# Kernel tuning notes

Measured on AMD Instinct MI355X. Metric: run time of the kernel, lower is better.

## Reference

```python
import jax, jax.numpy as jnp
import numpy as np

N_NODES = 100000
N_EDGES = 3200000
EMBED_DIM = 64


def setup_inputs() -> dict:
    key = jax.random.key(0)
    k1, k2, k3, k4 = jax.random.split(key, 4)
    x = jax.random.normal(k1, (N_NODES, EMBED_DIM), dtype=jnp.float32)
    adj_rows = jax.random.randint(k2, (N_EDGES,), 0, N_NODES, dtype=jnp.int64)
    adj_cols = jax.random.randint(k3, (N_EDGES,), 0, N_NODES, dtype=jnp.int64)
    adj_vals = jax.random.uniform(k4, (N_EDGES,), dtype=jnp.float32)
    return {"x": x, "adj_rows": adj_rows, "adj_cols": adj_cols, "adj_vals": adj_vals}


def reference(x, adj_rows, adj_cols, adj_vals):
    # out = adj @ x, adj sparse COO: out[r] += v * x[c] for each (r, c, v)
    messages = x[adj_cols] * adj_vals[:, None]          # [E, D]
    out = jax.ops.segment_sum(messages, adj_rows, num_segments=N_NODES)  # [N, D]
    return out
```

## Files before the change

kernel.cpp:

```cpp
#include <hip/hip_runtime.h>
#include <hip/hip_fp16.h>

#define EMBED_DIM 64
#define NBMAX 1024
#define RPB 128
#define RPB_SHIFT 7
#define CAP 6144
#define CHUNK 8192
#define SCAT_T 512
#define EPT (CHUNK / SCAT_T)
#define SENTINEL_KEY 0xFFFFFFFFu
#define SCAT_LDS (NBMAX * 4 * 3 + 512 * 4 + CHUNK * 8)

typedef float f32x8 __attribute__((ext_vector_type(8)));
typedef float f32x4 __attribute__((ext_vector_type(4)));

__device__ __forceinline__ int load_idx(const void* p, int e, bool i64) {
    return i64 ? (int)((const long long*)p)[e] : ((const int*)p)[e];
}

static inline size_t align_up(size_t v, size_t a) { return (v + a - 1) & ~(a - 1); }

__global__ __launch_bounds__(1024) void detect_zero_kernel(
    const unsigned int* __restrict__ rows_u32, int* __restrict__ flag,
    int* __restrict__ gcur, int nb) {
    const int tid = threadIdx.x;
    if (tid == 0) {
        int nz = 0;
        for (int i = 1; i < 128; i += 2) nz += (rows_u32[i] != 0u);
        *flag = (nz == 0) ? 1 : 0;
    }
    if (tid < nb) gcur[tid] = 0;
}

__global__ __launch_bounds__(256) void xconv_kernel(
    const float* __restrict__ x, ushort* __restrict__ xh, int n8) {
    int i = blockIdx.x * 256 + threadIdx.x;
    if (i >= n8) return;
    float4 a = ((const float4*)x)[i * 2];
    float4 b = ((const float4*)x)[i * 2 + 1];
    ushort h[8];
    h[0] = __half_as_ushort(__float2half_rn(a.x));
    h[1] = __half_as_ushort(__float2half_rn(a.y));
    h[2] = __half_as_ushort(__float2half_rn(a.z));
    h[3] = __half_as_ushort(__float2half_rn(a.w));
    h[4] = __half_as_ushort(__float2half_rn(b.x));
    h[5] = __half_as_ushort(__float2half_rn(b.y));
    h[6] = __half_as_ushort(__float2half_rn(b.z));
    h[7] = __half_as_ushort(__float2half_rn(b.w));
    ((uint4*)xh)[i] = *(const uint4*)h;
}

__global__ __launch_bounds__(SCAT_T) void bscatter_kernel(
    const void* __restrict__ rows_p, const void* __restrict__ cols_p,
    const float* __restrict__ vals, int* __restrict__ gcur,
    uint2* __restrict__ recs, const int* __restrict__ flag_p,
    int n_edges, int nb) {
    extern __shared__ char smem[];
    int*   h     = (int*)smem;
    int*   gbase = h + NBMAX;
    int*   lbase = gbase + NBMAX;
    int*   tsum  = lbase + NBMAX;
    uint2* rec   = (uint2*)(tsum + 512);

    const bool i64 = (*flag_p != 0);
    const int tid = threadIdx.x;
    const int c0e = blockIdx.x * CHUNK;
    int rloc[EPT];

    for (int i = tid; i < NBMAX; i += SCAT_T) h[i] = 0;
    __syncthreads();

    #pragma unroll
    for (int k = 0; k < EPT; ++k) {
        int e = c0e + k * SCAT_T + tid;
        int r = (e < n_edges) ? load_idx(rows_p, e, i64) : -1;
        rloc[k] = r;
        if (r >= 0) atomicAdd(&h[r >> RPB_SHIFT], 1);
    }
    __syncthreads();

    const int b0 = 2 * tid, b1 = 2 * tid + 1;
    int cb0 = h[b0], cb1 = h[b1];
    int s = cb0 + cb1;
    tsum[tid] = s;
    __syncthreads();
    for (int d = 1; d < 512; d <<= 1) {
        int u = (tid >= d) ? tsum[tid - d] : 0;
        __syncthreads();
        tsum[tid] += u;
        __syncthreads();
    }
    {
        int run = tsum[tid] - s;
        lbase[b0] = run;
        lbase[b1] = run + cb0;
        int a0 = (cb0 + 7) & ~7, a1 = (cb1 + 7) & ~7;
        gbase[b0] = cb0 ? (b0 * CAP + atomicAdd(&gcur[b0], a0)) : 0;
        gbase[b1] = cb1 ? (b1 * CAP + atomicAdd(&gcur[b1], a1)) : 0;
        h[b0] = 0;
        h[b1] = 0;
    }
    __syncthreads();

    #pragma unroll
    for (int k0 = 0; k0 < EPT; k0 += 4) {
        int cc[4]; float vv[4];
        #pragma unroll
        for (int j = 0; j < 4; ++j) {
            int e = c0e + (k0 + j) * SCAT_T + tid;
            if (rloc[k0 + j] >= 0) {
                cc[j] = load_idx(cols_p, e, i64);
                vv[j] = vals[e];
            }
        }
        #pragma unroll
        for (int j = 0; j < 4; ++j) {
            int r = rloc[k0 + j];
            if (r >= 0) {
                int b = r >> RPB_SHIFT;
                int pos = lbase[b] + atomicAdd(&h[b], 1);
                rec[pos] = make_uint2(
                    ((unsigned)(r & (RPB - 1)) << 20) | (unsigned)cc[j],
                    __float_as_uint(vv[j]));
            }
        }
    }
    __syncthreads();

    const int wave = tid >> 6, lane = tid & 63;
    for (int b = wave; b < nb; b += (SCAT_T / 64)) {
        int c = h[b];
        if (c == 0) continue;
        int ca = (c + 7) & ~7;
        int gb = gbase[b], lb = lbase[b];
        int lim = (b + 1) * CAP;
        for (int j = lane; j < ca; j += 64) {
            uint2 v = (j < c) ? rec[lb + j] : make_uint2(SENTINEL_KEY, 0u);
            int pos = gb + j;
            if (pos < lim) recs[pos] = v;
        }
    }
}

__global__ __launch_bounds__(512) void bsort_kernel(
    const int* __restrict__ gcur, const uint2* __restrict__ recs,
    uint2* __restrict__ recs2, uint2* __restrict__ srange, int N) {
    __shared__ int cnt[RPB];
    __shared__ int scn[RPB];
    __shared__ int rbase[RPB];
    const int b = blockIdx.x;
    const int tid = threadIdx.x;
    const int s = b * CAP;
    int n = gcur[b];
    if (n > CAP) n = CAP;

    if (tid < RPB) cnt[tid] = 0;
    __syncthreads();

    for (int i = tid; i < n; i += 512) {
        unsigned lr = recs[s + i].x >> 20;
        if (lr < RPB) atomicAdd(&cnt[lr], 1);
    }
    __syncthreads();

    if (tid < RPB) scn[tid] = cnt[tid];
    __syncthreads();
    for (int d = 1; d < RPB; d <<= 1) {
        int u = (tid < RPB && tid >= d) ? scn[tid - d] : 0;
        __syncthreads();
        if (tid < RPB) scn[tid] += u;
        __syncthreads();
    }
    if (tid < RPB) {
        int excl = scn[tid] - cnt[tid];
        rbase[tid] = excl;
        int row = b * RPB + tid;
        if (row < N) srange[row] = make_uint2(s + excl, s + excl + cnt[tid]);
        cnt[tid] = 0;
    }
    __syncthreads();

    for (int i = tid; i < n; i += 512) {
        uint2 e = recs[s + i];
        unsigned lr = e.x >> 20;
        if (lr < RPB) {
            int pos = s + rbase[lr] + atomicAdd(&cnt[lr], 1);
            recs2[pos] = make_uint2(e.x & 0xFFFFFu, e.y);
        }
    }
}

__global__ __launch_bounds__(256) void gather_kernel(
    const uint2* __restrict__ srange, const uint2* __restrict__ recs2,
    const ushort* __restrict__ xh, float* __restrict__ out, int N) {
    int t = blockIdx.x * blockDim.x + threadIdx.x;
    int row = t >> 3;
    if (row >= N) return;
    const int lane = t & 7;

    uint2 rg = srange[row];
    int e = (int)rg.x;
    const int e_end = (int)rg.y;
    f32x8 A = {};

    #define ACC8(U, V)                                                     \
        {                                                                  \
            float2 f0 = __half22float2(*(const __half2*)&(U).x);           \
            float2 f1 = __half22float2(*(const __half2*)&(U).y);           \
            float2 f2 = __half22float2(*(const __half2*)&(U).z);           \
            float2 f3 = __half22float2(*(const __half2*)&(U).w);           \
            A[0] += (V) * f0.x; A[1] += (V) * f0.y;                        \
            A[2] += (V) * f1.x; A[3] += (V) * f1.y;                        \
            A[4] += (V) * f2.x; A[5] += (V) * f2.y;                        \
            A[6] += (V) * f3.x; A[7] += (V) * f3.y;                        \
        }

    for (; e + 4 <= e_end; e += 4) {
        uint2 r0 = recs2[e],     r1 = recs2[e + 1];
        uint2 r2 = recs2[e + 2], r3 = recs2[e + 3];
        uint4 a0 = ((const uint4*)(xh + (size_t)r0.x * EMBED_DIM))[lane];
        uint4 a1 = ((const uint4*)(xh + (size_t)r1.x * EMBED_DIM))[lane];
        uint4 a2 = ((const uint4*)(xh + (size_t)r2.x * EMBED_DIM))[lane];
        uint4 a3 = ((const uint4*)(xh + (size_t)r3.x * EMBED_DIM))[lane];
        float v0 = __uint_as_float(r0.y), v1 = __uint_as_float(r1.y);
        float v2 = __uint_as_float(r2.y), v3 = __uint_as_float(r3.y);
        ACC8(a0, v0); ACC8(a1, v1); ACC8(a2, v2); ACC8(a3, v3);
    }
    for (; e < e_end; ++e) {
        uint2 r0 = recs2[e];
        uint4 a0 = ((const uint4*)(xh + (size_t)r0.x * EMBED_DIM))[lane];
        ACC8(a0, __uint_as_float(r0.y));
    }
    #undef ACC8

    f32x4 o0 = {A[0], A[1], A[2], A[3]};
    f32x4 o1 = {A[4], A[5], A[6], A[7]};
    f32x4* op = (f32x4*)(out + (size_t)row * EMBED_DIM) + lane * 2;
    __builtin_nontemporal_store(o0, op);
    __builtin_nontemporal_store(o1, op + 1);
}

__global__ __launch_bounds__(256) void spmv_coo_kernel(
    const void* __restrict__ rows_p, const void* __restrict__ cols_p,
    const float* __restrict__ vals, const float* __restrict__ x,
    float* __restrict__ out, const int* __restrict__ flag_p, int n_edges) {
    const bool i64 = (*flag_p != 0);
    const int lane16 = threadIdx.x & 15;
    long long t      = (long long)blockIdx.x * blockDim.x + threadIdx.x;
    long long stride = (long long)gridDim.x * blockDim.x;
    long long total  = (long long)n_edges * 16;
    for (; t < total; t += stride) {
        int e = (int)(t >> 4);
        int r = load_idx(rows_p, e, i64);
        int c = load_idx(cols_p, e, i64);
        float v = vals[e];
        float4 xv = ((const float4*)(x + (long long)c * EMBED_DIM))[lane16];
        float* o = out + (long long)r * EMBED_DIM + lane16 * 4;
        unsafeAtomicAdd(o + 0, xv.x * v);
        unsafeAtomicAdd(o + 1, xv.y * v);
        unsafeAtomicAdd(o + 2, xv.z * v);
        unsafeAtomicAdd(o + 3, xv.w * v);
    }
}

extern "C" void kernel_launch(void* const* d_in, const int* in_sizes, int n_in,
                              void* d_out, int out_size, void* d_ws, size_t ws_size,
                              hipStream_t stream) {
    const float* x    = (const float*)d_in[0];
    const void*  rows = d_in[1];
    const void*  cols = d_in[2];
    const float* vals = (const float*)d_in[3];
    float* out = (float*)d_out;
    const int E = in_sizes[1];
    const int N = out_size / EMBED_DIM;
    const int NB = (N + RPB - 1) >> RPB_SHIFT;

    char* ws = (char*)d_ws;
    size_t off = 0;
    int* flag = (int*)(ws + off);            off += 16;
    int* gcur = (int*)(ws + off);            off += (size_t)NBMAX * 4;
    off = align_up(off, 256);
    ushort* xh = (ushort*)(ws + off);        off += (size_t)N * EMBED_DIM * 2;
    off = align_up(off, 256);
    uint2* srange = (uint2*)(ws + off);      off += (size_t)N * 8;
    off = align_up(off, 256);
    uint2* recs = (uint2*)(ws + off);        off += (size_t)NB * CAP * 8;
    off = align_up(off, 256);
    uint2* recs2 = (uint2*)(ws + off);       off += (size_t)NB * CAP * 8;
    const size_t needed = off;

    if (ws_size < needed || NB > NBMAX || N > (1 << 20) ||
        (size_t)NB * CAP < (size_t)E / 2) {
        detect_zero_kernel<<<1, 1024, 0, stream>>>((const unsigned int*)rows,
                                                   flag, gcur, 0);
        (void)hipMemsetAsync(d_out, 0, (size_t)out_size * sizeof(float), stream);
        spmv_coo_kernel<<<8192, 256, 0, stream>>>(rows, cols, vals, x, out,
                                                  flag, E);
        return;
    }

    detect_zero_kernel<<<1, 1024, 0, stream>>>((const unsigned int*)rows,
                                               flag, gcur, NB);
    xconv_kernel<<<(N * 8 + 255) / 256, 256, 0, stream>>>(x, xh, N * 8);
    const int grid_c = (E + CHUNK - 1) / CHUNK;
    bscatter_kernel<<<grid_c, SCAT_T, SCAT_LDS, stream>>>(
        rows, cols, vals, gcur, recs, flag, E, NB);
    bsort_kernel<<<NB, 512, 0, stream>>>(gcur, recs, recs2, srange, N);
    const int grid_g = (N * 8 + 255) / 256;
    gather_kernel<<<grid_g, 256, 0, stream>>>(srange, recs2, xh, out, N);
}
```

Before: 159.9 us.

## Fuse flag detection into xconv, stage sort bucket in LDS, vectorize gather record loads

Merges the zero-flag detection and counter reset into the first block of the fp16 conversion kernel, removing one kernel launch. The bucket sort kernel now copies its bucket into LDS on the first pass, so the second pass reads LDS instead of re-reading global memory. The gather loop aligns to an even edge index and loads two records per 16-byte load. The costs are about 49KB of dynamic LDS per sort block, which can lower occupancy, and an extra peel iteration in the gather loop.

```diff
diff --git a/kernel.cpp b/kernel.cpp
--- a/kernel.cpp
+++ b/kernel.cpp
@@ -11,6 +11,7 @@
 #define EPT (CHUNK / SCAT_T)
 #define SENTINEL_KEY 0xFFFFFFFFu
 #define SCAT_LDS (NBMAX * 4 * 3 + 512 * 4 + CHUNK * 8)
+#define SORT_LDS (CAP * 8 + RPB * 4 * 3)
 
 typedef float f32x8 __attribute__((ext_vector_type(8)));
 typedef float f32x4 __attribute__((ext_vector_type(4)));
@@ -34,7 +35,17 @@
 }
 
 __global__ __launch_bounds__(256) void xconv_kernel(
-    const float* __restrict__ x, ushort* __restrict__ xh, int n8) {
+    const float* __restrict__ x, ushort* __restrict__ xh, int n8,
+    const unsigned int* __restrict__ rows_u32, int* __restrict__ flag,
+    int* __restrict__ gcur, int nb) {
+    if (blockIdx.x == 0) {
+        if (threadIdx.x == 0) {
+            int nz = 0;
+            for (int i = 1; i < 128; i += 2) nz += (rows_u32[i] != 0u);
+            *flag = (nz == 0) ? 1 : 0;
+        }
+        for (int j = threadIdx.x; j < nb; j += 256) gcur[j] = 0;
+    }
     int i = blockIdx.x * 256 + threadIdx.x;
     if (i >= n8) return;
     float4 a = ((const float4*)x)[i * 2];
@@ -146,9 +157,11 @@
 __global__ __launch_bounds__(512) void bsort_kernel(
     const int* __restrict__ gcur, const uint2* __restrict__ recs,
     uint2* __restrict__ recs2, uint2* __restrict__ srange, int N) {
-    __shared__ int cnt[RPB];
-    __shared__ int scn[RPB];
-    __shared__ int rbase[RPB];
+    extern __shared__ char smem[];
+    uint2* lrec  = (uint2*)smem;
+    int*   cnt   = (int*)(lrec + CAP);
+    int*   scn   = cnt + RPB;
+    int*   rbase = scn + RPB;
     const int b = blockIdx.x;
     const int tid = threadIdx.x;
     const int s = b * CAP;
@@ -159,7 +172,9 @@
     __syncthreads();
 
     for (int i = tid; i < n; i += 512) {
-        unsigned lr = recs[s + i].x >> 20;
+        uint2 v = recs[s + i];
+        lrec[i] = v;
+        unsigned lr = v.x >> 20;
         if (lr < RPB) atomicAdd(&cnt[lr], 1);
     }
     __syncthreads();
@@ -182,7 +197,7 @@
     __syncthreads();
 
     for (int i = tid; i < n; i += 512) {
-        uint2 e = recs[s + i];
+        uint2 e = lrec[i];
         unsigned lr = e.x >> 20;
         if (lr < RPB) {
             int pos = s + rbase[lr] + atomicAdd(&cnt[lr], 1);
@@ -215,23 +230,29 @@
             A[4] += (V) * f2.x; A[5] += (V) * f2.y;                        \
             A[6] += (V) * f3.x; A[7] += (V) * f3.y;                        \
         }
+    #define ACC1(E)                                                        \
+        {                                                                  \
+            uint2 r0 = recs2[E];                                           \
+            uint4 a0 = ((const uint4*)(xh + (size_t)r0.x * EMBED_DIM))[lane]; \
+            ACC8(a0, __uint_as_float(r0.y));                               \
+        }
+
+    if (e < e_end && (e & 1)) { ACC1(e); ++e; }
 
     for (; e + 4 <= e_end; e += 4) {
-        uint2 r0 = recs2[e],     r1 = recs2[e + 1];
-        uint2 r2 = recs2[e + 2], r3 = recs2[e + 3];
-        uint4 a0 = ((const uint4*)(xh + (size_t)r0.x * EMBED_DIM))[lane];
-        uint4 a1 = ((const uint4*)(xh + (size_t)r1.x * EMBED_DIM))[lane];
-        uint4 a2 = ((const uint4*)(xh + (size_t)r2.x * EMBED_DIM))[lane];
-        uint4 a3 = ((const uint4*)(xh + (size_t)r3.x * EMBED_DIM))[lane];
-        float v0 = __uint_as_float(r0.y), v1 = __uint_as_float(r1.y);
-        float v2 = __uint_as_float(r2.y), v3 = __uint_as_float(r3.y);
-        ACC8(a0, v0); ACC8(a1, v1); ACC8(a2, v2); ACC8(a3, v3);
-    }
-    for (; e < e_end; ++e) {
-        uint2 r0 = recs2[e];
-        uint4 a0 = ((const uint4*)(xh + (size_t)r0.x * EMBED_DIM))[lane];
-        ACC8(a0, __uint_as_float(r0.y));
-    }
+        uint4 p0 = *(const uint4*)(recs2 + e);
+        uint4 p1 = *(const uint4*)(recs2 + e + 2);
+        uint4 a0 = ((const uint4*)(xh + (size_t)p0.x * EMBED_DIM))[lane];
+        uint4 a1 = ((const uint4*)(xh + (size_t)p0.z * EMBED_DIM))[lane];
+        uint4 a2 = ((const uint4*)(xh + (size_t)p1.x * EMBED_DIM))[lane];
+        uint4 a3 = ((const uint4*)(xh + (size_t)p1.z * EMBED_DIM))[lane];
+        ACC8(a0, __uint_as_float(p0.y));
+        ACC8(a1, __uint_as_float(p0.w));
+        ACC8(a2, __uint_as_float(p1.y));
+        ACC8(a3, __uint_as_float(p1.w));
+    }
+    for (; e < e_end; ++e) ACC1(e);
+    #undef ACC1
     #undef ACC8
 
     f32x4 o0 = {A[0], A[1], A[2], A[3]};
@@ -300,13 +321,13 @@
         return;
     }
 
-    detect_zero_kernel<<<1, 1024, 0, stream>>>((const unsigned int*)rows,
-                                               flag, gcur, NB);
-    xconv_kernel<<<(N * 8 + 255) / 256, 256, 0, stream>>>(x, xh, N * 8);
+    const int n8 = N * 8;
+    xconv_kernel<<<(n8 + 255) / 256, 256, 0, stream>>>(
+        x, xh, n8, (const unsigned int*)rows, flag, gcur, NB);
     const int grid_c = (E + CHUNK - 1) / CHUNK;
     bscatter_kernel<<<grid_c, SCAT_T, SCAT_LDS, stream>>>(
         rows, cols, vals, gcur, recs, flag, E, NB);
-    bsort_kernel<<<NB, 512, 0, stream>>>(gcur, recs, recs2, srange, N);
+    bsort_kernel<<<NB, 512, SORT_LDS, stream>>>(gcur, recs, recs2, srange, N);
     const int grid_g = (N * 8 + 255) / 256;
     gather_kernel<<<grid_g, 256, 0, stream>>>(srange, recs2, xh, out, N);
 }
```

New measurement: 151.0 us. -5.5%, faster.
